# Kernel tuning notes

Measured on AMD Instinct MI355X. Metric: run time of the kernel, lower is better.

The kernel has to match this reference:

```python
import jax, jax.numpy as jnp
import numpy as np

N = 100000   # nodes
E = 1600000  # edges (avg degree 16)
F = 128      # num_features
H = 128      # hidden
BN_EPS = 1e-5
NORM_EPS = 1e-12


def setup_inputs() -> dict:
    key = jax.random.key(0)
    k = jax.random.split(key, 5)
    x = jax.random.normal(k[0], (N, F), dtype=jnp.float32)
    edge_index = jax.random.randint(k[1], (2, E), 0, N, dtype=jnp.int64)
    # Xavier-uniform linear weights (as in weights_init)
    s = float(np.sqrt(6.0 / (F + H)))
    W_l = jax.random.uniform(k[2], (F, H), jnp.float32, -s, s)  # neighbor branch
    b_l = jnp.zeros((H,), jnp.float32)
    W_r = jax.random.uniform(k[3], (F, H), jnp.float32, -s, s)  # root branch (no bias in PyG)
    gamma = jnp.ones((H,), jnp.float32)   # BatchNorm weight
    beta = jnp.zeros((H,), jnp.float32)   # BatchNorm bias
    return {"x": x, "edge_index": edge_index, "W_l": W_l, "b_l": b_l,
            "W_r": W_r, "gamma": gamma, "beta": beta}


def reference(x, edge_index, W_l, b_l, W_r, gamma, beta):
    n = x.shape[0]
    src, dst = edge_index[0], edge_index[1]
    # mean aggregation of neighbor messages x_j at destination nodes
    agg = jax.ops.segment_sum(x[src], dst, num_segments=n)                 # [N, F]
    deg = jax.ops.segment_sum(jnp.ones((src.shape[0],), x.dtype), dst,
                              num_segments=n)                              # [N]
    agg = agg / jnp.maximum(deg, 1.0)[:, None]
    # SAGEConv: lin_l(agg) + lin_r(x), then row-wise L2 normalize
    out = agg @ W_l + b_l + x @ W_r                                        # [N, H]
    nrm = jnp.sqrt(jnp.sum(out * out, axis=-1, keepdims=True))
    out = out / jnp.maximum(nrm, NORM_EPS)
    # transition: ReLU -> BatchNorm1d (batch stats, training mode) -> Dropout(identity)
    out = jax.nn.relu(out)
    mean = jnp.mean(out, axis=0)
    var = jnp.mean((out - mean) ** 2, axis=0)  # biased variance (torch BN)
    out = (out - mean) / jnp.sqrt(var + BN_EPS) * gamma + beta
    return out
```

## Files before the change

### kernel.cpp

```cpp
#include <hip/hip_runtime.h>
#include <hip/hip_bf16.h>

static constexpr int F = 128;
static constexpr int H = 128;
static constexpr int NPART = 128;

typedef __attribute__((ext_vector_type(8))) short short8;
typedef __attribute__((ext_vector_type(4))) float f32x4;

__device__ __forceinline__ unsigned short f2bf(float f) {
  union { float f; unsigned u; } a; a.f = f;
  unsigned r = a.u + 0x7FFF + ((a.u >> 16) & 1);
  return (unsigned short)(r >> 16);
}
__device__ __forceinline__ float bf2f(unsigned short h) {
  union { unsigned u; float f; } a; a.u = ((unsigned)h) << 16;
  return a.f;
}
__device__ __forceinline__ float bits2f(unsigned u) {
  union { unsigned u; float f; } a; a.u = u;
  return a.f;
}

__device__ __forceinline__ int detect64(const void* eiv) {
  const unsigned* u = (const unsigned*)eiv;
  int is64 = 1;
  for (int i = 0; i < 64; ++i) is64 &= (u[2 * i + 1] == 0u);
  return is64;
}

__global__ void detect_dtype(const unsigned* __restrict__ ei, int* __restrict__ flag) {
  if (blockIdx.x == 0 && threadIdx.x == 0) {
    int is64 = 1;
    for (int i = 0; i < 64; ++i) {
      if (ei[2 * i + 1] != 0u) { is64 = 0; break; }
    }
    *flag = is64;
  }
}

__device__ __forceinline__ int load_idx(const void* eiv, int is64, long long pos) {
  return is64 ? (int)((const long long*)eiv)[pos] : ((const int*)eiv)[pos];
}

__global__ __launch_bounds__(512) void part_hist(const void* __restrict__ eiv,
                                                 int* __restrict__ cmat,
                                                 int E, int nbuck, int chunk) {
  __shared__ int h[2048];
  const int t = threadIdx.x, b = blockIdx.x;
  for (int i = t; i < nbuck; i += 512) h[i] = 0;
  __syncthreads();
  int is64 = detect64(eiv);
  int s = b * chunk, e = min(E, s + chunk);
  for (int i = s + t; i < e; i += 512) {
    int dst = load_idx(eiv, is64, (long long)E + i);
    atomicAdd(&h[dst >> 6], 1);
  }
  __syncthreads();
  for (int i = t; i < nbuck; i += 512) cmat[i * NPART + b] = h[i];
}

__global__ __launch_bounds__(256) void scan1(const int* __restrict__ in,
                                             int* __restrict__ outx,
                                             int* __restrict__ blocksum, int n) {
  __shared__ int sm[256];
  int idx = blockIdx.x * 256 + threadIdx.x;
  int v = (idx < n) ? in[idx] : 0;
  sm[threadIdx.x] = v;
  __syncthreads();
  #pragma unroll
  for (int off = 1; off < 256; off <<= 1) {
    int t = (threadIdx.x >= off) ? sm[threadIdx.x - off] : 0;
    __syncthreads();
    sm[threadIdx.x] += t;
    __syncthreads();
  }
  if (idx < n) outx[idx] = sm[threadIdx.x] - v;
  if (threadIdx.x == 255) blocksum[blockIdx.x] = sm[255];
}

__global__ __launch_bounds__(1024) void scan2big(const int* __restrict__ blocksum,
                                                 int* __restrict__ blockoff, int nb) {
  __shared__ int sm[1024];
  int t = threadIdx.x;
  int v = (t < nb) ? blocksum[t] : 0;
  sm[t] = v;
  __syncthreads();
  for (int off = 1; off < 1024; off <<= 1) {
    int u = (t >= off) ? sm[t - off] : 0;
    __syncthreads();
    sm[t] += u;
    __syncthreads();
  }
  if (t < nb) blockoff[t] = sm[t] - v;
}

__global__ __launch_bounds__(256) void scan3p(int* __restrict__ obuf,
                                              const int* __restrict__ blockoff,
                                              int* __restrict__ bbase,
                                              float* __restrict__ colzero,
                                              int L, int nbuck, int E) {
  if (blockIdx.x == 0) colzero[threadIdx.x] = 0.0f;
  int idx = blockIdx.x * 256 + threadIdx.x;
  if (idx >= L) return;
  int v = obuf[idx] + blockoff[idx >> 8];
  obuf[idx] = v;
  if ((idx & (NPART - 1)) == 0) bbase[idx / NPART] = v;
  if (idx == 0) bbase[nbuck] = E;
}

__global__ __launch_bounds__(512) void part_scatter(const void* __restrict__ eiv,
                                                    const int* __restrict__ base,
                                                    int* __restrict__ ebuf,
                                                    int E, int nbuck, int chunk) {
  __shared__ int cur[2048];
  const int t = threadIdx.x, b = blockIdx.x;
  for (int i = t; i < nbuck; i += 512) cur[i] = base[i * NPART + b];
  __syncthreads();
  int is64 = detect64(eiv);
  int s = b * chunk, e = min(E, s + chunk);
  for (int i = s + t; i < e; i += 512) {
    int src = load_idx(eiv, is64, i);
    int dst = load_idx(eiv, is64, (long long)E + i);
    int pos = atomicAdd(&cur[dst >> 6], 1);
    ebuf[pos] = (src << 6) | (dst & 63);
  }
}

#define GCAP 2048
template <bool LOWP>
__global__ __launch_bounds__(256) void gather_bucket(
    const unsigned short* __restrict__ Y, const int* __restrict__ ebuf,
    const int* __restrict__ bbase, float* __restrict__ pio,
    const unsigned short* __restrict__ Pbf, unsigned short* __restrict__ Ubf,
    float* __restrict__ colsum, float* __restrict__ colsq, int n) {
  __shared__ int lsrc[GCAP];
  __shared__ int hist[65];
  __shared__ int loff[65];
  __shared__ int cur[64];
  __shared__ float csm[128], cqm[128];

  const int t = threadIdx.x;
  const int b = blockIdx.x;
  const int node0 = b << 6;
  const int s = bbase[b], e = bbase[b + 1];
  const int cnt = e - s;

  if (t < 65) hist[t] = 0;
  if (t < 128) { csm[t] = 0.f; cqm[t] = 0.f; }
  __syncthreads();

  const bool fast = (cnt <= GCAP);
  if (fast) {
    for (int i = s + t; i < e; i += 256)
      atomicAdd(&hist[ebuf[i] & 63], 1);
    __syncthreads();
    if (t < 64) loff[t] = hist[t];
    __syncthreads();
    #pragma unroll
    for (int off = 1; off < 64; off <<= 1) {
      int u = (t >= off && t < 64) ? loff[t - off] : 0;
      __syncthreads();
      if (t < 64) loff[t] += u;
      __syncthreads();
    }
    if (t < 64) cur[t] = loff[t] - hist[t];
    __syncthreads();
    for (int i = s + t; i < e; i += 256) {
      int p = ebuf[i];
      int pos = atomicAdd(&cur[p & 63], 1);
      lsrc[pos] = p >> 6;
    }
    __syncthreads();
  }

  const int lane = t & 63;
  const int w = t >> 6;
  const int half = lane >> 5;
  const int c = (lane & 31) * 4;

  float lcs[4] = {0.f, 0.f, 0.f, 0.f};
  float lcq[4] = {0.f, 0.f, 0.f, 0.f};

  #pragma unroll
  for (int it = 0; it < 8; ++it) {
    int ln = it * 8 + w * 2 + half;
    int node = node0 + ln;
    if (node >= n) continue;
    int ls, le;
    if (fast) { ls = loff[ln] - hist[ln]; le = loff[ln]; }
    else      { ls = 0; le = 0; }

    float acc[8][4];
    #pragma unroll
    for (int u = 0; u < 8; ++u)
      #pragma unroll
      for (int q = 0; q < 4; ++q) acc[u][q] = 0.0f;

    int j = ls;
    for (; j + 7 < le; j += 8) {
      #pragma unroll
      for (int u = 0; u < 8; ++u) {
        int sj = lsrc[j + u];
        uint2 uv = *(const uint2*)(Y + (size_t)sj * H + c);
        acc[u][0] += bits2f(uv.x << 16);
        acc[u][1] += bits2f(uv.x & 0xFFFF0000u);
        acc[u][2] += bits2f(uv.y << 16);
        acc[u][3] += bits2f(uv.y & 0xFFFF0000u);
      }
    }
    for (; j + 1 < le; j += 2) {
      #pragma unroll
      for (int u = 0; u < 2; ++u) {
        int sj = lsrc[j + u];
        uint2 uv = *(const uint2*)(Y + (size_t)sj * H + c);
        acc[u][0] += bits2f(uv.x << 16);
        acc[u][1] += bits2f(uv.x & 0xFFFF0000u);
        acc[u][2] += bits2f(uv.y << 16);
        acc[u][3] += bits2f(uv.y & 0xFFFF0000u);
      }
    }
    if (j < le) {
      int sj = lsrc[j];
      uint2 uv = *(const uint2*)(Y + (size_t)sj * H + c);
      acc[0][0] += bits2f(uv.x << 16);
      acc[0][1] += bits2f(uv.x & 0xFFFF0000u);
      acc[0][2] += bits2f(uv.y << 16);
      acc[0][3] += bits2f(uv.y & 0xFFFF0000u);
    }

    float deg = 0.0f;
    float a0, a1, a2, a3;
    if (fast) {
      deg = (float)(le - ls);
      #pragma unroll
      for (int u = 4; u < 8; ++u) {
        acc[u - 4][0] += acc[u][0]; acc[u - 4][1] += acc[u][1];
        acc[u - 4][2] += acc[u][2]; acc[u - 4][3] += acc[u][3];
      }
      a0 = (acc[0][0] + acc[1][0]) + (acc[2][0] + acc[3][0]);
      a1 = (acc[0][1] + acc[1][1]) + (acc[2][1] + acc[3][1]);
      a2 = (acc[0][2] + acc[1][2]) + (acc[2][2] + acc[3][2]);
      a3 = (acc[0][3] + acc[1][3]) + (acc[2][3] + acc[3][3]);
    } else {
      a0 = a1 = a2 = a3 = 0.0f;
      for (int jj = s; jj < e; ++jj) {
        int p = ebuf[jj];
        if ((p & 63) == ln) {
          deg += 1.0f;
          uint2 uv = *(const uint2*)(Y + (size_t)(p >> 6) * H + c);
          a0 += bits2f(uv.x << 16);
          a1 += bits2f(uv.x & 0xFFFF0000u);
          a2 += bits2f(uv.y << 16);
          a3 += bits2f(uv.y & 0xFFFF0000u);
        }
      }
    }

    float inv = 1.0f / fmaxf(deg, 1.0f);
    float p0, p1, p2, p3;
    if (LOWP) {
      uint2 pv = *(const uint2*)(Pbf + (size_t)node * H + c);
      p0 = bits2f(pv.x << 16);
      p1 = bits2f(pv.x & 0xFFFF0000u);
      p2 = bits2f(pv.y << 16);
      p3 = bits2f(pv.y & 0xFFFF0000u);
    } else {
      float4 p = *(const float4*)(pio + (size_t)node * H + c);
      p0 = p.x; p1 = p.y; p2 = p.z; p3 = p.w;
    }
    float v0 = p0 + a0 * inv;
    float v1 = p1 + a1 * inv;
    float v2 = p2 + a2 * inv;
    float v3 = p3 + a3 * inv;
    float sq = v0 * v0 + v1 * v1 + v2 * v2 + v3 * v3;
    sq += __shfl_xor(sq, 1, 64);
    sq += __shfl_xor(sq, 2, 64);
    sq += __shfl_xor(sq, 4, 64);
    sq += __shfl_xor(sq, 8, 64);
    sq += __shfl_xor(sq, 16, 64);
    float rs = 1.0f / fmaxf(sqrtf(sq), 1e-12f);
    float u0 = fmaxf(v0 * rs, 0.f), u1 = fmaxf(v1 * rs, 0.f);
    float u2 = fmaxf(v2 * rs, 0.f), u3 = fmaxf(v3 * rs, 0.f);
    if (LOWP) {
      uint2 ov;
      ov.x = (unsigned)f2bf(u0) | ((unsigned)f2bf(u1) << 16);
      ov.y = (unsigned)f2bf(u2) | ((unsigned)f2bf(u3) << 16);
      *(uint2*)(Ubf + (size_t)node * H + c) = ov;
    } else {
      float4 o = {u0, u1, u2, u3};
      *(float4*)(pio + (size_t)node * H + c) = o;
    }
    lcs[0] += u0; lcq[0] += u0 * u0;
    lcs[1] += u1; lcq[1] += u1 * u1;
    lcs[2] += u2; lcq[2] += u2 * u2;
    lcs[3] += u3; lcq[3] += u3 * u3;
  }

  #pragma unroll
  for (int q = 0; q < 4; ++q) {
    atomicAdd(&csm[c + q], lcs[q]);
    atomicAdd(&cqm[c + q], lcq[q]);
  }
  __syncthreads();
  if (t < 128) {
    atomicAdd(&colsum[t], csm[t]);
    atomicAdd(&colsq[t], cqm[t]);
  }
}

__global__ __launch_bounds__(256) void deg_count(const void* __restrict__ eiv,
                                                 const int* __restrict__ flag,
                                                 int* __restrict__ degi, int E) {
  int e = blockIdx.x * blockDim.x + threadIdx.x;
  if (e >= E) return;
  int dst = load_idx(eiv, *flag, (long long)E + e);
  atomicAdd(&degi[dst], 1);
}

__global__ __launch_bounds__(256) void scan3(int* __restrict__ offsets,
                                             const int* __restrict__ blockoff,
                                             int* __restrict__ cursor, int n, int E) {
  int idx = blockIdx.x * 256 + threadIdx.x;
  if (idx >= n) return;
  int off = offsets[idx] + blockoff[idx >> 8];
  offsets[idx] = off;
  cursor[idx] = off;
  if (idx == 0) offsets[n] = E;
}

__global__ __launch_bounds__(256) void bucket_fill(const void* __restrict__ eiv,
                                                   const int* __restrict__ flag,
                                                   int* __restrict__ cursor,
                                                   int* __restrict__ csr_src, int E) {
  int e = blockIdx.x * blockDim.x + threadIdx.x;
  if (e >= E) return;
  int is64 = *flag;
  int src = load_idx(eiv, is64, e);
  int dst = load_idx(eiv, is64, (long long)E + e);
  int pos = atomicAdd(&cursor[dst], 1);
  csr_src[pos] = src;
}

__global__ __launch_bounds__(256) void prep_w(const float* __restrict__ Wl,
                                              const float* __restrict__ Wr,
                                              unsigned short* __restrict__ Wcat) {
  int tid = blockIdx.x * 256 + threadIdx.x;
  if (tid >= 4 * 4 * 8 * 64) return;
  int lane = tid & 63;
  int nf   = (tid >> 6) & 7;
  int kc   = (tid >> 9) & 3;
  int part = tid >> 11;
  const float* W = (part < 2) ? Wl : Wr;
  bool lo = (part & 1);
  int ncol = nf * 16 + (lane & 15);
  int k0 = kc * 32 + (lane >> 4) * 8;
  unsigned short ov[8];
  #pragma unroll
  for (int j = 0; j < 8; ++j) {
    float v = W[(k0 + j) * H + ncol];
    unsigned short h = f2bf(v);
    ov[j] = lo ? f2bf(v - bf2f(h)) : h;
  }
  uint4 pack;
  pack.x = (unsigned)ov[0] | ((unsigned)ov[1] << 16);
  pack.y = (unsigned)ov[2] | ((unsigned)ov[3] << 16);
  pack.z = (unsigned)ov[4] | ((unsigned)ov[5] << 16);
  pack.w = (unsigned)ov[6] | ((unsigned)ov[7] << 16);
  *(uint4*)(Wcat + (size_t)tid * 8) = pack;
}

template <bool LOWP>
__global__ __launch_bounds__(256) void dual_gemm(
    const float* __restrict__ x, const unsigned short* __restrict__ Wcat,
    const float* __restrict__ bl, unsigned short* __restrict__ Y,
    float* __restrict__ pout, unsigned short* __restrict__ Pbf, int n) {
  __shared__ unsigned short As[2][64][128];

  const int t = threadIdx.x;
  const int i0 = blockIdx.x * 64;

  #pragma unroll
  for (int it = 0; it < 8; ++it) {
    int idx = it * 256 + t;
    int r = idx >> 5;
    int c4 = (idx & 31) * 4;
    int row_g = i0 + r; if (row_g >= n) row_g = n - 1;
    int boff = (((c4 >> 3) ^ (r & 7)) << 3) + (c4 & 7);
    float4 vx = *(const float4*)(x + (size_t)row_g * F + c4);
    unsigned short h0 = f2bf(vx.x), h1 = f2bf(vx.y), h2 = f2bf(vx.z), h3 = f2bf(vx.w);
    uint2 hv = { (unsigned)h0 | ((unsigned)h1 << 16), (unsigned)h2 | ((unsigned)h3 << 16) };
    *(uint2*)&As[0][r][boff] = hv;
    unsigned short l0 = f2bf(vx.x - bf2f(h0)), l1 = f2bf(vx.y - bf2f(h1));
    unsigned short l2 = f2bf(vx.z - bf2f(h2)), l3 = f2bf(vx.w - bf2f(h3));
    uint2 lv = { (unsigned)l0 | ((unsigned)l1 << 16), (unsigned)l2 | ((unsigned)l3 << 16) };
    *(uint2*)&As[1][r][boff] = lv;
  }
  __syncthreads();

  const int w = t >> 6;
  const int lane = t & 63;

  f32x4 accL[4][2], accR[4][2];
  #pragma unroll
  for (int rf = 0; rf < 4; ++rf)
    #pragma unroll
    for (int nfi = 0; nfi < 2; ++nfi) {
      accL[rf][nfi] = (f32x4){0.f, 0.f, 0.f, 0.f};
      accR[rf][nfi] = (f32x4){0.f, 0.f, 0.f, 0.f};
    }

  const int APM[3] = {0, 1, 0};
  const int BL[3]  = {0, 0, 1};
  const int BR[3]  = {2, 2, 3};

  #pragma unroll
  for (int pass = 0; pass < 3; ++pass) {
    const int ap = APM[pass];
    #pragma unroll
    for (int kc = 0; kc < 4; ++kc) {
      short8 afr[4];
      int chunk = kc * 4 + (lane >> 4);
      #pragma unroll
      for (int rf = 0; rf < 4; ++rf) {
        int row = rf * 16 + (lane & 15);
        afr[rf] = *(const short8*)(&As[ap][row][(chunk ^ (row & 7)) * 8]);
      }
      short8 bfrL[2], bfrR[2];
      #pragma unroll
      for (int nfi = 0; nfi < 2; ++nfi) {
        int blobL = (BL[pass] * 4 + kc) * 8 + (w * 2 + nfi);
        int blobR = (BR[pass] * 4 + kc) * 8 + (w * 2 + nfi);
        bfrL[nfi] = *(const short8*)(Wcat + (size_t)blobL * 512 + lane * 8);
        bfrR[nfi] = *(const short8*)(Wcat + (size_t)blobR * 512 + lane * 8);
      }
      #pragma unroll
      for (int rf = 0; rf < 4; ++rf)
        #pragma unroll
        for (int nfi = 0; nfi < 2; ++nfi) {
          accL[rf][nfi] = __builtin_amdgcn_mfma_f32_16x16x32_bf16(
              afr[rf], bfrL[nfi], accL[rf][nfi], 0, 0, 0);
          accR[rf][nfi] = __builtin_amdgcn_mfma_f32_16x16x32_bf16(
              afr[rf], bfrR[nfi], accR[rf][nfi], 0, 0, 0);
        }
    }
  }

  const float b0 = bl[w * 32 + (lane & 15)];
  const float b1 = bl[w * 32 + 16 + (lane & 15)];

  #pragma unroll
  for (int rf = 0; rf < 4; ++rf) {
    #pragma unroll
    for (int r4 = 0; r4 < 4; ++r4) {
      int rl = rf * 16 + (lane >> 4) * 4 + r4;
      int row = i0 + rl;
      if (row < n) {
        Y[(size_t)row * H + w * 32 + (lane & 15)]      = f2bf(accL[rf][0][r4]);
        Y[(size_t)row * H + w * 32 + 16 + (lane & 15)] = f2bf(accL[rf][1][r4]);
        if (LOWP) {
          Pbf[(size_t)row * H + w * 32 + (lane & 15)]      = f2bf(accR[rf][0][r4] + b0);
          Pbf[(size_t)row * H + w * 32 + 16 + (lane & 15)] = f2bf(accR[rf][1][r4] + b1);
        } else {
          pout[(size_t)row * H + w * 32 + (lane & 15)]      = accR[rf][0][r4] + b0;
          pout[(size_t)row * H + w * 32 + 16 + (lane & 15)] = accR[rf][1][r4] + b1;
        }
      }
    }
  }
}

__global__ __launch_bounds__(256) void gather_mean(const float* __restrict__ x,
                                                   const int* __restrict__ offsets,
                                                   const int* __restrict__ csr_src,
                                                   float* __restrict__ out, int n) {
  int node = (int)(((long long)blockIdx.x * blockDim.x + threadIdx.x) >> 6);
  int lane = threadIdx.x & 63;
  if (node >= n) return;
  int s = offsets[node], e = offsets[node + 1];
  float ax = 0.0f, ay = 0.0f, bx = 0.0f, by = 0.0f;
  int j = s;
  for (; j + 1 < e; j += 2) {
    int s0 = csr_src[j], s1 = csr_src[j + 1];
    float2 v0 = *(const float2*)(x + (size_t)s0 * F + lane * 2);
    float2 v1 = *(const float2*)(x + (size_t)s1 * F + lane * 2);
    ax += v0.x; ay += v0.y;
    bx += v1.x; by += v1.y;
  }
  if (j < e) {
    int s0 = csr_src[j];
    float2 v0 = *(const float2*)(x + (size_t)s0 * F + lane * 2);
    ax += v0.x; ay += v0.y;
  }
  float inv = 1.0f / fmaxf((float)(e - s), 1.0f);
  float2 r; r.x = (ax + bx) * inv; r.y = (ay + by) * inv;
  *(float2*)(out + (size_t)node * H + lane * 2) = r;
}

__global__ __launch_bounds__(256) void mfma_gemm(
    const float* __restrict__ x, const unsigned short* __restrict__ Wcat,
    const float* __restrict__ bl, float* __restrict__ out,
    float* __restrict__ colsum, float* __restrict__ colsq, int n) {
  __shared__ unsigned short As[4][64][128];
  __shared__ float rowsq[64][4];
  __shared__ float rscale[64];

  const int t = threadIdx.x;
  const int i0 = blockIdx.x * 64;

  #pragma unroll
  for (int it = 0; it < 8; ++it) {
    int idx = it * 256 + t;
    int r = idx >> 5;
    int c4 = (idx & 31) * 4;
    int row_g = i0 + r; if (row_g >= n) row_g = n - 1;
    int boff = (((c4 >> 3) ^ (r & 7)) << 3) + (c4 & 7);
    float4 va = *(const float4*)(out + (size_t)row_g * H + c4);
    float4 vx = *(const float4*)(x + (size_t)row_g * H + c4);
    unsigned short h0 = f2bf(va.x), h1 = f2bf(va.y), h2 = f2bf(va.z), h3 = f2bf(va.w);
    uint2 hv = { (unsigned)h0 | ((unsigned)h1 << 16), (unsigned)h2 | ((unsigned)h3 << 16) };
    *(uint2*)&As[0][r][boff] = hv;
    unsigned short l0 = f2bf(va.x - bf2f(h0)), l1 = f2bf(va.y - bf2f(h1));
    unsigned short l2 = f2bf(va.z - bf2f(h2)), l3 = f2bf(va.w - bf2f(h3));
    uint2 lv = { (unsigned)l0 | ((unsigned)l1 << 16), (unsigned)l2 | ((unsigned)l3 << 16) };
    *(uint2*)&As[1][r][boff] = lv;
    h0 = f2bf(vx.x); h1 = f2bf(vx.y); h2 = f2bf(vx.z); h3 = f2bf(vx.w);
    uint2 hx = { (unsigned)h0 | ((unsigned)h1 << 16), (unsigned)h2 | ((unsigned)h3 << 16) };
    *(uint2*)&As[2][r][boff] = hx;
    l0 = f2bf(vx.x - bf2f(h0)); l1 = f2bf(vx.y - bf2f(h1));
    l2 = f2bf(vx.z - bf2f(h2)); l3 = f2bf(vx.w - bf2f(h3));
    uint2 lx = { (unsigned)l0 | ((unsigned)l1 << 16), (unsigned)l2 | ((unsigned)l3 << 16) };
    *(uint2*)&As[3][r][boff] = lx;
  }
  __syncthreads();

  const int w = t >> 6;
  const int lane = t & 63;

  f32x4 acc[4][2];
  #pragma unroll
  for (int rf = 0; rf < 4; ++rf)
    #pragma unroll
    for (int nfi = 0; nfi < 2; ++nfi)
      acc[rf][nfi] = (f32x4){0.f, 0.f, 0.f, 0.f};

  const int APM[6] = {0, 1, 0, 2, 3, 2};
  const int BPM[6] = {0, 0, 1, 2, 2, 3};

  #pragma unroll
  for (int pass = 0; pass < 6; ++pass) {
    const int ap = APM[pass], bp = BPM[pass];
    #pragma unroll
    for (int kc = 0; kc < 4; ++kc) {
      short8 bfr[2];
      #pragma unroll
      for (int nfi = 0; nfi < 2; ++nfi) {
        int blob = (bp * 4 + kc) * 8 + (w * 2 + nfi);
        bfr[nfi] = *(const short8*)(Wcat + (size_t)blob * 512 + lane * 8);
      }
      short8 afr[4];
      int chunk = kc * 4 + (lane >> 4);
      #pragma unroll
      for (int rf = 0; rf < 4; ++rf) {
        int row = rf * 16 + (lane & 15);
        afr[rf] = *(const short8*)(&As[ap][row][(chunk ^ (row & 7)) * 8]);
      }
      #pragma unroll
      for (int rf = 0; rf < 4; ++rf)
        #pragma unroll
        for (int nfi = 0; nfi < 2; ++nfi)
          acc[rf][nfi] = __builtin_amdgcn_mfma_f32_16x16x32_bf16(
              afr[rf], bfr[nfi], acc[rf][nfi], 0, 0, 0);
    }
  }

  const float b0 = bl[w * 32 + (lane & 15)];
  const float b1 = bl[w * 32 + 16 + (lane & 15)];

  #pragma unroll
  for (int rf = 0; rf < 4; ++rf) {
    #pragma unroll
    for (int r4 = 0; r4 < 4; ++r4) {
      float v0 = acc[rf][0][r4] + b0;
      float v1 = acc[rf][1][r4] + b1;
      acc[rf][0][r4] = v0;
      acc[rf][1][r4] = v1;
      float sq = v0 * v0 + v1 * v1;
      sq += __shfl_xor(sq, 1, 64);
      sq += __shfl_xor(sq, 2, 64);
      sq += __shfl_xor(sq, 4, 64);
      sq += __shfl_xor(sq, 8, 64);
      if ((lane & 15) == 0) rowsq[rf * 16 + (lane >> 4) * 4 + r4][w] = sq;
    }
  }
  __syncthreads();
  if (t < 64) {
    float s = rowsq[t][0] + rowsq[t][1] + rowsq[t][2] + rowsq[t][3];
    rscale[t] = 1.0f / fmaxf(sqrtf(s), 1e-12f);
  }
  __syncthreads();

  float cs0 = 0.f, cq0 = 0.f, cs1 = 0.f, cq1 = 0.f;
  #pragma unroll
  for (int rf = 0; rf < 4; ++rf) {
    #pragma unroll
    for (int r4 = 0; r4 < 4; ++r4) {
      int rl = rf * 16 + (lane >> 4) * 4 + r4;
      int row = i0 + rl;
      float s = rscale[rl];
      float u0 = fmaxf(acc[rf][0][r4] * s, 0.f);
      float u1 = fmaxf(acc[rf][1][r4] * s, 0.f);
      if (row < n) {
        out[(size_t)row * H + w * 32 + (lane & 15)] = u0;
        out[(size_t)row * H + w * 32 + 16 + (lane & 15)] = u1;
        cs0 += u0; cq0 += u0 * u0;
        cs1 += u1; cq1 += u1 * u1;
      }
    }
  }
  cs0 += __shfl_xor(cs0, 16, 64); cs0 += __shfl_xor(cs0, 32, 64);
  cq0 += __shfl_xor(cq0, 16, 64); cq0 += __shfl_xor(cq0, 32, 64);
  cs1 += __shfl_xor(cs1, 16, 64); cs1 += __shfl_xor(cs1, 32, 64);
  cq1 += __shfl_xor(cq1, 16, 64); cq1 += __shfl_xor(cq1, 32, 64);
  if (lane < 16) {
    atomicAdd(&colsum[w * 32 + lane], cs0);
    atomicAdd(&colsq[w * 32 + lane], cq0);
    atomicAdd(&colsum[w * 32 + 16 + lane], cs1);
    atomicAdd(&colsq[w * 32 + 16 + lane], cq1);
  }
}

__global__ __launch_bounds__(256) void scatter_mean(
    const float* __restrict__ x, const void* __restrict__ eiv,
    const int* __restrict__ flag, float* __restrict__ agg,
    float* __restrict__ deg, int E) {
  long long gid = (long long)blockIdx.x * blockDim.x + threadIdx.x;
  int e = (int)(gid >> 5);
  int ch = (int)(gid & 31);
  if (e >= E) return;
  int is64 = *flag;
  int src = load_idx(eiv, is64, e);
  int dst = load_idx(eiv, is64, (long long)E + e);
  float4 v = *(const float4*)(x + (size_t)src * F + ch * 4);
  float* a = agg + (size_t)dst * H + ch * 4;
  atomicAdd(a + 0, v.x);
  atomicAdd(a + 1, v.y);
  atomicAdd(a + 2, v.z);
  atomicAdd(a + 3, v.w);
  if (ch == 0) atomicAdd(deg + dst, 1.0f);
}

__global__ __launch_bounds__(256) void divide_deg(float* __restrict__ out,
                                                  const float* __restrict__ deg,
                                                  long long n4) {
  long long i = (long long)blockIdx.x * blockDim.x + threadIdx.x;
  if (i >= n4) return;
  int node = (int)(i >> 5);
  float s = 1.0f / fmaxf(deg[node], 1.0f);
  float4 v = ((float4*)out)[i];
  v.x *= s; v.y *= s; v.z *= s; v.w *= s;
  ((float4*)out)[i] = v;
}

__global__ __launch_bounds__(256) void fused_gemm(
    const float* __restrict__ x, const float* __restrict__ Wl,
    const float* __restrict__ bl, const float* __restrict__ Wr,
    float* __restrict__ out, float* __restrict__ colsum, float* __restrict__ colsq) {
  __shared__ float As[16][256];
  __shared__ float rp[4][8];
  __shared__ float rscale[16];
  __shared__ float cs[128], cs2[128];

  const int t = threadIdx.x;
  const int i0 = blockIdx.x * 16;

  #pragma unroll
  for (int it = 0; it < 2; ++it) {
    int idx = (it * 256 + t) * 4;
    int r = idx >> 7, c = idx & 127;
    float4 va = *(const float4*)(out + (size_t)(i0 + r) * H + c);
    As[r][c + 0] = va.x; As[r][c + 1] = va.y;
    As[r][c + 2] = va.z; As[r][c + 3] = va.w;
    float4 vx = *(const float4*)(x + (size_t)(i0 + r) * F + c);
    As[r][128 + c + 0] = vx.x; As[r][128 + c + 1] = vx.y;
    As[r][128 + c + 2] = vx.z; As[r][128 + c + 3] = vx.w;
  }
  __syncthreads();

  const int c = t & 127;
  const int half = t >> 7;
  float acc[8];
  #pragma unroll
  for (int r = 0; r < 8; ++r) acc[r] = 0.0f;

  #pragma unroll 4
  for (int k = 0; k < 128; ++k) {
    float w = Wl[k * H + c];
    #pragma unroll
    for (int r = 0; r < 8; ++r) acc[r] = fmaf(As[half * 8 + r][k], w, acc[r]);
  }
  #pragma unroll 4
  for (int k = 0; k < 128; ++k) {
    float w = Wr[k * H + c];
    #pragma unroll
    for (int r = 0; r < 8; ++r) acc[r] = fmaf(As[half * 8 + r][128 + k], w, acc[r]);
  }
  const float bias = bl[c];
  #pragma unroll
  for (int r = 0; r < 8; ++r) acc[r] += bias;

  float sq[8];
  #pragma unroll
  for (int r = 0; r < 8; ++r) sq[r] = acc[r] * acc[r];
  #pragma unroll
  for (int off = 32; off > 0; off >>= 1) {
    #pragma unroll
    for (int r = 0; r < 8; ++r) sq[r] += __shfl_down(sq[r], off, 64);
  }
  const int wv = t >> 6;
  if ((t & 63) == 0) {
    #pragma unroll
    for (int r = 0; r < 8; ++r) rp[wv][r] = sq[r];
  }
  __syncthreads();
  if (t < 16) {
    int base = (t >> 3) * 2, rr = t & 7;
    float s = rp[base][rr] + rp[base + 1][rr];
    rscale[t] = 1.0f / fmaxf(sqrtf(s), 1e-12f);
  }
  __syncthreads();

  float csum = 0.0f, csq = 0.0f;
  #pragma unroll
  for (int r = 0; r < 8; ++r) {
    float v = fmaxf(acc[r] * rscale[half * 8 + r], 0.0f);
    out[(size_t)(i0 + half * 8 + r) * H + c] = v;
    csum += v;
    csq += v * v;
  }
  if (half == 1) { cs[c] = csum; cs2[c] = csq; }
  __syncthreads();
  if (half == 0) {
    atomicAdd(&colsum[c], csum + cs[c]);
    atomicAdd(&colsq[c], csq + cs2[c]);
  }
}

__global__ void bn_stats(const float* __restrict__ colsum, const float* __restrict__ colsq,
                         const float* __restrict__ gamma, const float* __restrict__ beta,
                         float* __restrict__ scale, float* __restrict__ shift, int n) {
  int c = threadIdx.x;
  if (c < H) {
    float inv_n = 1.0f / (float)n;
    float mean = colsum[c] * inv_n;
    float var = colsq[c] * inv_n - mean * mean;
    float istd = rsqrtf(var + 1e-5f);
    float sc = gamma[c] * istd;
    scale[c] = sc;
    shift[c] = beta[c] - mean * sc;
  }
}

__global__ __launch_bounds__(256) void bn_apply(
    float* __restrict__ out, const float* __restrict__ scale,
    const float* __restrict__ shift, long long n4) {
  long long i = (long long)blockIdx.x * blockDim.x + threadIdx.x;
  if (i >= n4) return;
  float4 v = ((float4*)out)[i];
  int c = (int)((i * 4) & (H - 1));
  v.x = fmaf(v.x, scale[c + 0], shift[c + 0]);
  v.y = fmaf(v.y, scale[c + 1], shift[c + 1]);
  v.z = fmaf(v.z, scale[c + 2], shift[c + 2]);
  v.w = fmaf(v.w, scale[c + 3], shift[c + 3]);
  ((float4*)out)[i] = v;
}

__global__ __launch_bounds__(256) void bn_apply_lo(
    const unsigned short* __restrict__ U, float* __restrict__ out,
    const float* __restrict__ scale, const float* __restrict__ shift,
    long long n4) {
  long long i = (long long)blockIdx.x * blockDim.x + threadIdx.x;
  if (i >= n4) return;
  uint2 uv = ((const uint2*)U)[i];
  int c = (int)((i * 4) & (H - 1));
  float4 v;
  v.x = fmaf(bits2f(uv.x << 16),          scale[c + 0], shift[c + 0]);
  v.y = fmaf(bits2f(uv.x & 0xFFFF0000u),  scale[c + 1], shift[c + 1]);
  v.z = fmaf(bits2f(uv.y << 16),          scale[c + 2], shift[c + 2]);
  v.w = fmaf(bits2f(uv.y & 0xFFFF0000u),  scale[c + 3], shift[c + 3]);
  ((float4*)out)[i] = v;
}

extern "C" void kernel_launch(void* const* d_in, const int* in_sizes, int n_in,
                              void* d_out, int out_size, void* d_ws, size_t ws_size,
                              hipStream_t stream) {
  const float* x     = (const float*)d_in[0];
  const void*  ei    = d_in[1];
  const float* Wl    = (const float*)d_in[2];
  const float* bl    = (const float*)d_in[3];
  const float* Wr    = (const float*)d_in[4];
  const float* gamma = (const float*)d_in[5];
  const float* beta  = (const float*)d_in[6];
  float* out = (float*)d_out;

  const int n = in_sizes[0] / F;
  const int E = in_sizes[1] / 2;
  const int nb = (n + 255) / 256;
  const int nbuck = (n + 63) >> 6;

  char* ws = (char*)d_ws;
  int* flag = (int*)ws;
  unsigned short* Wcat = (unsigned short*)(ws + 256);
  char* after_w = ws + 256 + 4 * 128 * 128 * 2;

  int*   cmat    = (int*)after_w;
  int*   obuf    = cmat + 2048 * NPART;
  int*   bsum    = obuf + 2048 * NPART;
  int*   boff    = bsum + 1024;
  int*   bbase   = boff + 1024;
  float* fcs     = (float*)(bbase + 2049);
  float* fcq     = fcs + H;
  float* fsc     = fcq + H;
  float* fsh     = fsc + H;
  int*   ebuf    = (int*)(fsh + H);
  unsigned short* Yws = (unsigned short*)(ebuf + E);
  unsigned short* Pws = Yws + (size_t)n * H;
  unsigned short* Uws = Pws + (size_t)n * H;
  size_t need_fast  = (size_t)((char*)(Yws + (size_t)n * H) - ws);
  size_t need_fast2 = (size_t)((char*)(Uws + (size_t)n * H) - ws);

  int*   degi     = (int*)after_w;
  int*   offsets  = degi + n;
  int*   cursor   = offsets + n + 1;
  int*   blocksum = cursor + n;
  int*   blockoff = blocksum + nb;
  float* mcs      = (float*)(blockoff + nb);
  float* mcq      = mcs + H;
  float* msc      = mcq + H;
  float* msh      = msc + H;
  int*   csr_src  = (int*)(msh + H);
  size_t need_mid = (size_t)((char*)(csr_src + E) - ws);

  float *colsum, *colsq, *scale, *shift;

  const int eb = (E + 255) / 256;
  const int gb = (n + 63) / 64;
  const long long n4 = (long long)n * H / 4;

  if (ws_size >= need_fast && nbuck <= 2048) {
    const bool lowp = (ws_size >= need_fast2);
    colsum = fcs; colsq = fcq; scale = fsc; shift = fsh;

    prep_w<<<32, 256, 0, stream>>>(Wl, Wr, Wcat);
    if (lowp)
      dual_gemm<true><<<gb, 256, 0, stream>>>(x, Wcat, bl, Yws, out, Pws, n);
    else
      dual_gemm<false><<<gb, 256, 0, stream>>>(x, Wcat, bl, Yws, out, Pws, n);

    const int chunk = (E + NPART - 1) / NPART;
    const int L = nbuck * NPART;
    const int nb2 = (L + 255) / 256;
    part_hist<<<NPART, 512, 0, stream>>>(ei, cmat, E, nbuck, chunk);
    scan1<<<nb2, 256, 0, stream>>>(cmat, obuf, bsum, L);
    scan2big<<<1, 1024, 0, stream>>>(bsum, boff, nb2);
    scan3p<<<nb2, 256, 0, stream>>>(obuf, boff, bbase, colsum, L, nbuck, E);
    part_scatter<<<NPART, 512, 0, stream>>>(ei, obuf, ebuf, E, nbuck, chunk);

    if (lowp)
      gather_bucket<true><<<nbuck, 256, 0, stream>>>(
          Yws, ebuf, bbase, out, Pws, Uws, colsum, colsq, n);
    else
      gather_bucket<false><<<nbuck, 256, 0, stream>>>(
          Yws, ebuf, bbase, out, Pws, Uws, colsum, colsq, n);

    bn_stats<<<1, 128, 0, stream>>>(colsum, colsq, gamma, beta, scale, shift, n);
    if (lowp)
      bn_apply_lo<<<(int)((n4 + 255) / 256), 256, 0, stream>>>(
          Uws, out, scale, shift, n4);
    else
      bn_apply<<<(int)((n4 + 255) / 256), 256, 0, stream>>>(out, scale, shift, n4);
  } else if (ws_size >= need_mid) {
    colsum = mcs; colsq = mcq; scale = msc; shift = msh;
    detect_dtype<<<1, 64, 0, stream>>>((const unsigned*)ei, flag);
    hipMemsetAsync(degi, 0, (size_t)n * 4, stream);
    hipMemsetAsync(colsum, 0, 2 * H * 4, stream);

    prep_w<<<32, 256, 0, stream>>>(Wl, Wr, Wcat);

    deg_count<<<eb, 256, 0, stream>>>(ei, flag, degi, E);
    scan1<<<nb, 256, 0, stream>>>(degi, offsets, blocksum, n);
    scan2big<<<1, 1024, 0, stream>>>(blocksum, blockoff, nb);
    scan3<<<nb, 256, 0, stream>>>(offsets, blockoff, cursor, n, E);
    bucket_fill<<<eb, 256, 0, stream>>>(ei, flag, cursor, csr_src, E);

    long long gthreads = (long long)n * 64;
    gather_mean<<<(int)((gthreads + 255) / 256), 256, 0, stream>>>(
        x, offsets, csr_src, out, n);

    mfma_gemm<<<gb, 256, 0, stream>>>(x, Wcat, bl, out, colsum, colsq, n);
    bn_stats<<<1, 128, 0, stream>>>(colsum, colsq, gamma, beta, scale, shift, n);
    bn_apply<<<(int)((n4 + 255) / 256), 256, 0, stream>>>(out, scale, shift, n4);
  } else {
    float* deg = (float*)(ws + 256);
    colsum = deg + n; colsq = colsum + H; scale = colsq + H; shift = scale + H;
    detect_dtype<<<1, 64, 0, stream>>>((const unsigned*)ei, flag);
    hipMemsetAsync(d_out, 0, (size_t)out_size * sizeof(float), stream);
    hipMemsetAsync(deg, 0, (size_t)n * 4 + 4 * H * 4, stream);
    long long sthreads = (long long)E * 32;
    scatter_mean<<<(int)((sthreads + 255) / 256), 256, 0, stream>>>(x, ei, flag, out, deg, E);
    long long n4f = (long long)n * H / 4;
    divide_deg<<<(int)((n4f + 255) / 256), 256, 0, stream>>>(out, deg, n4f);
    fused_gemm<<<n / 16, 256, 0, stream>>>(x, Wl, bl, Wr, out, colsum, colsq);
    bn_stats<<<1, 128, 0, stream>>>(colsum, colsq, gamma, beta, scale, shift, n);
    bn_apply<<<(int)((n4 + 255) / 256), 256, 0, stream>>>(out, scale, shift, n4);
  }
}
```

Before: 231.0 us.

## Split each 64-node gather bucket across two blocks with 16-byte row loads

The gather kernel now launches two blocks per 64-node bucket, and each block handles 32 destination nodes. Both blocks scan the full bucket edge list and keep only their half. Each node is now processed by 16 lanes loading 8 bf16 values (uint4) instead of 32 lanes loading 4, which halves the shuffle reduction depth and widens memory transactions. The intent is more blocks for occupancy and fewer, wider gather loads. In exchange, each edge list is read twice and the per-thread register footprint grows.

```diff
diff --git a/kernel.cpp b/kernel.cpp
--- a/kernel.cpp
+++ b/kernel.cpp
@@ -129,178 +129,214 @@
 
 #define GCAP 2048
 template <bool LOWP>
-__global__ __launch_bounds__(256) void gather_bucket(
+__global__ __launch_bounds__(256) void gather_half(
     const unsigned short* __restrict__ Y, const int* __restrict__ ebuf,
     const int* __restrict__ bbase, float* __restrict__ pio,
     const unsigned short* __restrict__ Pbf, unsigned short* __restrict__ Ubf,
     float* __restrict__ colsum, float* __restrict__ colsq, int n) {
   __shared__ int lsrc[GCAP];
-  __shared__ int hist[65];
-  __shared__ int loff[65];
-  __shared__ int cur[64];
+  __shared__ int hist[32];
+  __shared__ int loff[32];
+  __shared__ int cur[32];
   __shared__ float csm[128], cqm[128];
 
   const int t = threadIdx.x;
-  const int b = blockIdx.x;
-  const int node0 = b << 6;
+  const int blk = blockIdx.x;
+  const int b = blk >> 1;
+  const int hb = blk & 1;
+  const int node0 = (b << 6) + (hb << 5);
   const int s = bbase[b], e = bbase[b + 1];
-  const int cnt = e - s;
-
-  if (t < 65) hist[t] = 0;
+
+  if (t < 32) hist[t] = 0;
   if (t < 128) { csm[t] = 0.f; cqm[t] = 0.f; }
   __syncthreads();
 
-  const bool fast = (cnt <= GCAP);
+  for (int i = s + t; i < e; i += 256) {
+    int ln = (ebuf[i] & 63) - (hb << 5);
+    if ((unsigned)ln < 32u) atomicAdd(&hist[ln], 1);
+  }
+  __syncthreads();
+  if (t < 32) loff[t] = hist[t];
+  __syncthreads();
+  #pragma unroll
+  for (int off = 1; off < 32; off <<= 1) {
+    int u = (t >= off && t < 32) ? loff[t - off] : 0;
+    __syncthreads();
+    if (t < 32) loff[t] += u;
+    __syncthreads();
+  }
+  if (t < 32) cur[t] = loff[t] - hist[t];
+  __syncthreads();
+  const bool fast = (loff[31] <= GCAP);
   if (fast) {
-    for (int i = s + t; i < e; i += 256)
-      atomicAdd(&hist[ebuf[i] & 63], 1);
-    __syncthreads();
-    if (t < 64) loff[t] = hist[t];
-    __syncthreads();
-    #pragma unroll
-    for (int off = 1; off < 64; off <<= 1) {
-      int u = (t >= off && t < 64) ? loff[t - off] : 0;
-      __syncthreads();
-      if (t < 64) loff[t] += u;
-      __syncthreads();
-    }
-    if (t < 64) cur[t] = loff[t] - hist[t];
-    __syncthreads();
     for (int i = s + t; i < e; i += 256) {
       int p = ebuf[i];
-      int pos = atomicAdd(&cur[p & 63], 1);
-      lsrc[pos] = p >> 6;
+      int ln = (p & 63) - (hb << 5);
+      if ((unsigned)ln < 32u) {
+        int pos = atomicAdd(&cur[ln], 1);
+        lsrc[pos] = p >> 6;
+      }
     }
     __syncthreads();
   }
 
   const int lane = t & 63;
   const int w = t >> 6;
-  const int half = lane >> 5;
-  const int c = (lane & 31) * 4;
-
-  float lcs[4] = {0.f, 0.f, 0.f, 0.f};
-  float lcq[4] = {0.f, 0.f, 0.f, 0.f};
-
-  #pragma unroll
-  for (int it = 0; it < 8; ++it) {
-    int ln = it * 8 + w * 2 + half;
+  const int g = lane >> 4;
+  const int c8 = (lane & 15) * 8;
+
+  float lcs[8], lcq[8];
+  #pragma unroll
+  for (int q = 0; q < 8; ++q) { lcs[q] = 0.f; lcq[q] = 0.f; }
+
+  #pragma unroll
+  for (int it = 0; it < 2; ++it) {
+    int ln = it * 16 + w * 4 + g;
     int node = node0 + ln;
     if (node >= n) continue;
-    int ls, le;
-    if (fast) { ls = loff[ln] - hist[ln]; le = loff[ln]; }
-    else      { ls = 0; le = 0; }
-
-    float acc[8][4];
-    #pragma unroll
-    for (int u = 0; u < 8; ++u)
+
+    float a[8];
+    #pragma unroll
+    for (int q = 0; q < 8; ++q) a[q] = 0.f;
+    float deg = 0.0f;
+
+    if (fast) {
+      int ls = loff[ln] - hist[ln];
+      int le = loff[ln];
+      deg = (float)(le - ls);
+      float acc[8][8];
       #pragma unroll
-      for (int q = 0; q < 4; ++q) acc[u][q] = 0.0f;
-
-    int j = ls;
-    for (; j + 7 < le; j += 8) {
+      for (int u = 0; u < 8; ++u)
+        #pragma unroll
+        for (int q = 0; q < 8; ++q) acc[u][q] = 0.f;
+
+      int j = ls;
+      for (; j + 7 < le; j += 8) {
+        #pragma unroll
+        for (int u = 0; u < 8; ++u) {
+          int sj = lsrc[j + u];
+          uint4 uv = *(const uint4*)(Y + (size_t)sj * H + c8);
+          acc[u][0] += bits2f(uv.x << 16);
+          acc[u][1] += bits2f(uv.x & 0xFFFF0000u);
+          acc[u][2] += bits2f(uv.y << 16);
+          acc[u][3] += bits2f(uv.y & 0xFFFF0000u);
+          acc[u][4] += bits2f(uv.z << 16);
+          acc[u][5] += bits2f(uv.z & 0xFFFF0000u);
+          acc[u][6] += bits2f(uv.w << 16);
+          acc[u][7] += bits2f(uv.w & 0xFFFF0000u);
+        }
+      }
+      for (; j + 1 < le; j += 2) {
+        #pragma unroll
+        for (int u = 0; u < 2; ++u) {
+          int sj = lsrc[j + u];
+          uint4 uv = *(const uint4*)(Y + (size_t)sj * H + c8);
+          acc[u][0] += bits2f(uv.x << 16);
+          acc[u][1] += bits2f(uv.x & 0xFFFF0000u);
+          acc[u][2] += bits2f(uv.y << 16);
+          acc[u][3] += bits2f(uv.y & 0xFFFF0000u);
+          acc[u][4] += bits2f(uv.z << 16);
+          acc[u][5] += bits2f(uv.z & 0xFFFF0000u);
+          acc[u][6] += bits2f(uv.w << 16);
+          acc[u][7] += bits2f(uv.w & 0xFFFF0000u);
+        }
+      }
+      if (j < le) {
+        int sj = lsrc[j];
+        uint4 uv = *(const uint4*)(Y + (size_t)sj * H + c8);
+        acc[0][0] += bits2f(uv.x << 16);
+        acc[0][1] += bits2f(uv.x & 0xFFFF0000u);
+        acc[0][2] += bits2f(uv.y << 16);
+        acc[0][3] += bits2f(uv.y & 0xFFFF0000u);
+        acc[0][4] += bits2f(uv.z << 16);
+        acc[0][5] += bits2f(uv.z & 0xFFFF0000u);
+        acc[0][6] += bits2f(uv.w << 16);
+        acc[0][7] += bits2f(uv.w & 0xFFFF0000u);
+      }
       #pragma unroll
-      for (int u = 0; u < 8; ++u) {
-        int sj = lsrc[j + u];
-        uint2 uv = *(const uint2*)(Y + (size_t)sj * H + c);
-        acc[u][0] += bits2f(uv.x << 16);
-        acc[u][1] += bits2f(uv.x & 0xFFFF0000u);
-        acc[u][2] += bits2f(uv.y << 16);
-        acc[u][3] += bits2f(uv.y & 0xFFFF0000u);
-      }
-    }
-    for (; j + 1 < le; j += 2) {
+      for (int u = 4; u < 8; ++u)
+        #pragma unroll
+        for (int q = 0; q < 8; ++q) acc[u - 4][q] += acc[u][q];
       #pragma unroll
-      for (int u = 0; u < 2; ++u) {
-        int sj = lsrc[j + u];
-        uint2 uv = *(const uint2*)(Y + (size_t)sj * H + c);
-        acc[u][0] += bits2f(uv.x << 16);
-        acc[u][1] += bits2f(uv.x & 0xFFFF0000u);
-        acc[u][2] += bits2f(uv.y << 16);
-        acc[u][3] += bits2f(uv.y & 0xFFFF0000u);
-      }
-    }
-    if (j < le) {
-      int sj = lsrc[j];
-      uint2 uv = *(const uint2*)(Y + (size_t)sj * H + c);
-      acc[0][0] += bits2f(uv.x << 16);
-      acc[0][1] += bits2f(uv.x & 0xFFFF0000u);
-      acc[0][2] += bits2f(uv.y << 16);
-      acc[0][3] += bits2f(uv.y & 0xFFFF0000u);
-    }
-
-    float deg = 0.0f;
-    float a0, a1, a2, a3;
-    if (fast) {
-      deg = (float)(le - ls);
-      #pragma unroll
-      for (int u = 4; u < 8; ++u) {
-        acc[u - 4][0] += acc[u][0]; acc[u - 4][1] += acc[u][1];
-        acc[u - 4][2] += acc[u][2]; acc[u - 4][3] += acc[u][3];
-      }
-      a0 = (acc[0][0] + acc[1][0]) + (acc[2][0] + acc[3][0]);
-      a1 = (acc[0][1] + acc[1][1]) + (acc[2][1] + acc[3][1]);
-      a2 = (acc[0][2] + acc[1][2]) + (acc[2][2] + acc[3][2]);
-      a3 = (acc[0][3] + acc[1][3]) + (acc[2][3] + acc[3][3]);
+      for (int q = 0; q < 8; ++q)
+        a[q] = (acc[0][q] + acc[1][q]) + (acc[2][q] + acc[3][q]);
     } else {
-      a0 = a1 = a2 = a3 = 0.0f;
+      int lnfull = ln + (hb << 5);
       for (int jj = s; jj < e; ++jj) {
         int p = ebuf[jj];
-        if ((p & 63) == ln) {
+        if ((p & 63) == lnfull) {
           deg += 1.0f;
-          uint2 uv = *(const uint2*)(Y + (size_t)(p >> 6) * H + c);
-          a0 += bits2f(uv.x << 16);
-          a1 += bits2f(uv.x & 0xFFFF0000u);
-          a2 += bits2f(uv.y << 16);
-          a3 += bits2f(uv.y & 0xFFFF0000u);
+          uint4 uv = *(const uint4*)(Y + (size_t)(p >> 6) * H + c8);
+          a[0] += bits2f(uv.x << 16);
+          a[1] += bits2f(uv.x & 0xFFFF0000u);
+          a[2] += bits2f(uv.y << 16);
+          a[3] += bits2f(uv.y & 0xFFFF0000u);
+          a[4] += bits2f(uv.z << 16);
+          a[5] += bits2f(uv.z & 0xFFFF0000u);
+          a[6] += bits2f(uv.w << 16);
+          a[7] += bits2f(uv.w & 0xFFFF0000u);
         }
       }
     }
 
     float inv = 1.0f / fmaxf(deg, 1.0f);
-    float p0, p1, p2, p3;
+    float v[8];
     if (LOWP) {
-      uint2 pv = *(const uint2*)(Pbf + (size_t)node * H + c);
-      p0 = bits2f(pv.x << 16);
-      p1 = bits2f(pv.x & 0xFFFF0000u);
-      p2 = bits2f(pv.y << 16);
-      p3 = bits2f(pv.y & 0xFFFF0000u);
+      uint4 pv = *(const uint4*)(Pbf + (size_t)node * H + c8);
+      v[0] = bits2f(pv.x << 16)         + a[0] * inv;
+      v[1] = bits2f(pv.x & 0xFFFF0000u) + a[1] * inv;
+      v[2] = bits2f(pv.y << 16)         + a[2] * inv;
+      v[3] = bits2f(pv.y & 0xFFFF0000u) + a[3] * inv;
+      v[4] = bits2f(pv.z << 16)         + a[4] * inv;
+      v[5] = bits2f(pv.z & 0xFFFF0000u) + a[5] * inv;
+      v[6] = bits2f(pv.w << 16)         + a[6] * inv;
+      v[7] = bits2f(pv.w & 0xFFFF0000u) + a[7] * inv;
     } else {
-      float4 p = *(const float4*)(pio + (size_t)node * H + c);
-      p0 = p.x; p1 = p.y; p2 = p.z; p3 = p.w;
-    }
-    float v0 = p0 + a0 * inv;
-    float v1 = p1 + a1 * inv;
-    float v2 = p2 + a2 * inv;
-    float v3 = p3 + a3 * inv;
-    float sq = v0 * v0 + v1 * v1 + v2 * v2 + v3 * v3;
+      float4 pa = *(const float4*)(pio + (size_t)node * H + c8);
+      float4 pb = *(const float4*)(pio + (size_t)node * H + c8 + 4);
+      v[0] = pa.x + a[0] * inv; v[1] = pa.y + a[1] * inv;
+      v[2] = pa.z + a[2] * inv; v[3] = pa.w + a[3] * inv;
+      v[4] = pb.x + a[4] * inv; v[5] = pb.y + a[5] * inv;
+      v[6] = pb.z + a[6] * inv; v[7] = pb.w + a[7] * inv;
+    }
+
+    float sq = 0.f;
+    #pragma unroll
+    for (int q = 0; q < 8; ++q) sq += v[q] * v[q];
     sq += __shfl_xor(sq, 1, 64);
     sq += __shfl_xor(sq, 2, 64);
     sq += __shfl_xor(sq, 4, 64);
     sq += __shfl_xor(sq, 8, 64);
-    sq += __shfl_xor(sq, 16, 64);
     float rs = 1.0f / fmaxf(sqrtf(sq), 1e-12f);
-    float u0 = fmaxf(v0 * rs, 0.f), u1 = fmaxf(v1 * rs, 0.f);
-    float u2 = fmaxf(v2 * rs, 0.f), u3 = fmaxf(v3 * rs, 0.f);
+
+    float u_[8];
+    #pragma unroll
+    for (int q = 0; q < 8; ++q) u_[q] = fmaxf(v[q] * rs, 0.f);
+
     if (LOWP) {
-      uint2 ov;
-      ov.x = (unsigned)f2bf(u0) | ((unsigned)f2bf(u1) << 16);
-      ov.y = (unsigned)f2bf(u2) | ((unsigned)f2bf(u3) << 16);
-      *(uint2*)(Ubf + (size_t)node * H + c) = ov;
+      uint4 ov;
+      ov.x = (unsigned)f2bf(u_[0]) | ((unsigned)f2bf(u_[1]) << 16);
+      ov.y = (unsigned)f2bf(u_[2]) | ((unsigned)f2bf(u_[3]) << 16);
+      ov.z = (unsigned)f2bf(u_[4]) | ((unsigned)f2bf(u_[5]) << 16);
+      ov.w = (unsigned)f2bf(u_[6]) | ((unsigned)f2bf(u_[7]) << 16);
+      *(uint4*)(Ubf + (size_t)node * H + c8) = ov;
     } else {
-      float4 o = {u0, u1, u2, u3};
-      *(float4*)(pio + (size_t)node * H + c) = o;
-    }
-    lcs[0] += u0; lcq[0] += u0 * u0;
-    lcs[1] += u1; lcq[1] += u1 * u1;
-    lcs[2] += u2; lcq[2] += u2 * u2;
-    lcs[3] += u3; lcq[3] += u3 * u3;
-  }
-
-  #pragma unroll
-  for (int q = 0; q < 4; ++q) {
-    atomicAdd(&csm[c + q], lcs[q]);
-    atomicAdd(&cqm[c + q], lcq[q]);
+      float4 oa = {u_[0], u_[1], u_[2], u_[3]};
+      float4 ob = {u_[4], u_[5], u_[6], u_[7]};
+      *(float4*)(pio + (size_t)node * H + c8) = oa;
+      *(float4*)(pio + (size_t)node * H + c8 + 4) = ob;
+    }
+    #pragma unroll
+    for (int q = 0; q < 8; ++q) {
+      lcs[q] += u_[q];
+      lcq[q] += u_[q] * u_[q];
+    }
+  }
+
+  #pragma unroll
+  for (int q = 0; q < 8; ++q) {
+    atomicAdd(&csm[c8 + q], lcs[q]);
+    atomicAdd(&cqm[c8 + q], lcq[q]);
   }
   __syncthreads();
   if (t < 128) {
@@ -867,10 +903,10 @@
     part_scatter<<<NPART, 512, 0, stream>>>(ei, obuf, ebuf, E, nbuck, chunk);
 
     if (lowp)
-      gather_bucket<true><<<nbuck, 256, 0, stream>>>(
+      gather_half<true><<<2 * nbuck, 256, 0, stream>>>(
           Yws, ebuf, bbase, out, Pws, Uws, colsum, colsq, n);
     else
-      gather_bucket<false><<<nbuck, 256, 0, stream>>>(
+      gather_half<false><<<2 * nbuck, 256, 0, stream>>>(
           Yws, ebuf, bbase, out, Pws, Uws, colsum, colsq, n);
 
     bn_stats<<<1, 128, 0, stream>>>(colsum, colsq, gamma, beta, scale, shift, n);
```

Result: slower. 265.4 us (+14.9%).
